# Optimization experiments

Hardware: AMD Instinct MI355X
Metric: run time of the kernel (lower is better)

## Reference

```python
import jax, jax.numpy as jnp
import numpy as np

EPS = 1e-5  # BatchNorm eps (inference-mode BN with running stats)


def bn(x, g, b, m, v):
    # x: [B,C,H,W]; per-channel affine BN (inference)
    inv = jax.lax.rsqrt(v + EPS)
    return (x - m[None, :, None, None]) * (g * inv)[None, :, None, None] + b[None, :, None, None]


def conv1x1(x, w):
    # x: [B,Ci,H,W], w: [Co,Ci,1,1]
    return jnp.einsum('bchw,oc->bohw', x, w[:, :, 0, 0])


def conv3x3(x, w, b):
    out = jax.lax.conv_general_dilated(
        x, w, window_strides=(1, 1), padding=((1, 1), (1, 1)),
        dimension_numbers=('NCHW', 'OIHW', 'NCHW'))
    return out + b[None, :, None, None]


def deform_conv3x3(x, offset, w):
    # x: [B,C,H,W]; offset: [B,18,H,W] with channel 2k = dy_k, 2k+1 = dx_k
    # w: [Co,C,3,3]; stride=1, pad=1, dilation=1, deformable_groups=1
    B, C, H, W = x.shape
    K = 9
    kidx = jnp.arange(K)
    kdy = (kidx // 3 - 1).astype(x.dtype)  # base kernel y offsets in {-1,0,1}
    kdx = (kidx % 3 - 1).astype(x.dtype)
    off = offset.reshape(B, K, 2, H, W)
    gh = jnp.arange(H, dtype=x.dtype)
    gw = jnp.arange(W, dtype=x.dtype)
    # sampling locations [B,K,H,W]
    py = gh[None, None, :, None] + kdy[None, :, None, None] + off[:, :, 0]
    px = gw[None, None, None, :] + kdx[None, :, None, None] + off[:, :, 1]

    y0 = jnp.floor(py)
    x0 = jnp.floor(px)
    wy1 = py - y0
    wx1 = px - x0
    y0i = y0.astype(jnp.int32)
    x0i = x0.astype(jnp.int32)

    xflat = x.reshape(B, C, H * W)

    def gather(yi, xi):
        valid = ((yi >= 0) & (yi < H) & (xi >= 0) & (xi < W))
        idx = (jnp.clip(yi, 0, H - 1) * W + jnp.clip(xi, 0, W - 1)).reshape(B, 1, -1)
        g = jnp.take_along_axis(xflat, idx, axis=2).reshape(B, C, K, H, W)
        return g * valid[:, None].astype(x.dtype)

    sampled = (
        gather(y0i, x0i) * ((1 - wy1) * (1 - wx1))[:, None]
        + gather(y0i, x0i + 1) * ((1 - wy1) * wx1)[:, None]
        + gather(y0i + 1, x0i) * (wy1 * (1 - wx1))[:, None]
        + gather(y0i + 1, x0i + 1) * (wy1 * wx1)[:, None]
    )  # [B,C,K,H,W]
    return jnp.einsum('bckhw,ock->bohw', sampled, w.reshape(w.shape[0], C, K))


def setup_inputs() -> dict:
    key = jax.random.key(0)
    ks = jax.random.split(key, 20)
    B, Cin, H, W = 2, 1024, 64, 64
    Cb, Cout = 256, 1024

    def msra(k, shape):
        fan_out = shape[0] * int(np.prod(shape[2:]))
        return jax.random.normal(k, shape, jnp.float32) * np.sqrt(2.0 / fan_out)

    inp = {
        'x': jax.random.normal(ks[0], (B, Cin, H, W), jnp.float32),
        'w1': msra(ks[1], (Cb, Cin, 1, 1)),
        'g1': jnp.ones((Cb,)), 'b1': jnp.zeros((Cb,)),
        'm1': jax.random.normal(ks[2], (Cb,)) * 0.1,
        'v1': jax.random.uniform(ks[3], (Cb,)) + 0.5,
        # offset conv (small weights so offsets stay in a realistic range)
        'w_off': msra(ks[4], (18, Cb, 3, 3)) * 0.05,
        'b_off': jnp.zeros((18,)),
        'w2': msra(ks[5], (Cb, Cb, 3, 3)),
        'g2': jnp.ones((Cb,)), 'b2': jnp.zeros((Cb,)),
        'm2': jax.random.normal(ks[6], (Cb,)) * 0.1,
        'v2': jax.random.uniform(ks[7], (Cb,)) + 0.5,
        'w3': msra(ks[8], (Cout, Cb, 1, 1)),
        'g3': jnp.ones((Cout,)), 'b3': jnp.zeros((Cout,)),
        'm3': jax.random.normal(ks[9], (Cout,)) * 0.1,
        'v3': jax.random.uniform(ks[10], (Cout,)) + 0.5,
    }
    return inp


def reference(x, w1, g1, b1, m1, v1, w_off, b_off, w2, g2, b2, m2, v2,
              w3, g3, b3, m3, v3):
    out = jax.nn.relu(bn(conv1x1(x, w1), g1, b1, m1, v1))
    offset = conv3x3(out, w_off, b_off)          # [B,18,H,W]
    out = bn(deform_conv3x3(out, offset, w2), g2, b2, m2, v2)
    out = jax.nn.relu(out)
    out = bn(conv1x1(out, w3), g3, b3, m3, v3)
    out = out + x                                 # identity shortcut (Cin==Cout, stride=1)
    return jax.nn.relu(out)
```

## Files before the change

kernel.cpp:

```cpp
#include <hip/hip_runtime.h>
#include <hip/hip_bf16.h>

#define EPSV 1e-5f

typedef __attribute__((ext_vector_type(4))) float f32x4;
typedef __attribute__((ext_vector_type(8))) short bf16x8;
typedef unsigned short u16;
typedef unsigned int u32;

#define AS1(p) ((const __attribute__((address_space(1))) void*)(p))
#define AS3(p) ((__attribute__((address_space(3))) void*)(p))

__device__ __forceinline__ float bf2f(u16 u) {
    union { u32 i; float f; } x; x.i = ((u32)u) << 16; return x.f;
}
__device__ __forceinline__ u16 f2bf(float f) {
    __hip_bfloat16 h = __float2bfloat16(f);
    return *reinterpret_cast<u16*>(&h);
}

__global__ __launch_bounds__(256) void prep_cvt(const float* __restrict__ w1,
                                                const float* __restrict__ w3,
                                                u16* __restrict__ wb1,
                                                u16* __restrict__ wb3) {
    int i = blockIdx.x * 256 + threadIdx.x;
    const float* src; u16* dst; int j;
    if (i < 65536) { src = w1; dst = wb1; j = i; }
    else           { src = w3; dst = wb3; j = i - 65536; }
    float4 v = ((const float4*)src)[j];
    ushort4 o;
    o.x = f2bf(v.x); o.y = f2bf(v.y); o.z = f2bf(v.z); o.w = f2bf(v.w);
    ((ushort4*)dst)[j] = o;
}

__global__ __launch_bounds__(256) void prep_reorg(const float* __restrict__ w_off,
                                                  const float* __restrict__ w2,
                                                  u16* __restrict__ wOffP,
                                                  u16* __restrict__ wb2p,
                                                  u16* __restrict__ zbuf) {
    const int bz = blockIdx.x;
    const int c  = threadIdx.x;
    if (bz == 320) { ((u32*)zbuf)[c] = 0; return; }
    const float* src; u16* dst; int o, O;
    if (bz < 64) { o = bz;      O = 18;  src = w_off; dst = wOffP; }
    else         { o = bz - 64; O = 256; src = w2;    dst = wb2p;  }
#pragma unroll
    for (int k = 0; k < 9; k++) {
        float v = (o < O) ? src[((size_t)(o * 256 + c)) * 9 + k] : 0.f;
        dst[(size_t)o * 2304 + k * 256 + c] = f2bf(v);
    }
}

__global__ __launch_bounds__(256) void cvt_x_T(const float* __restrict__ x,
                                               u16* __restrict__ xbT) {
    __shared__ u16 tile[64][72];
    const int tid = threadIdx.x;
    const int hw0 = blockIdx.x << 6;
    const int c0  = blockIdx.y << 6;
    const int b   = blockIdx.z;
    const int cl  = tid >> 4;
    const int hwl = (tid & 15) << 2;
#pragma unroll
    for (int i = 0; i < 4; i++) {
        const int c = cl + i * 16;
        float4 v = *(const float4*)(x + (((size_t)(b * 1024 + c0 + c)) << 12) + hw0 + hwl);
        tile[hwl + 0][c] = f2bf(v.x);
        tile[hwl + 1][c] = f2bf(v.y);
        tile[hwl + 2][c] = f2bf(v.z);
        tile[hwl + 3][c] = f2bf(v.w);
    }
    __syncthreads();
    const int hw  = tid >> 2;
    const int seg = tid & 3;
    u16* dst = xbT + ((size_t)(b * 4096 + hw0 + hw)) * 1024 + c0 + seg * 16;
    const u16* src = &tile[hw][seg * 16];
#pragma unroll
    for (int q = 0; q < 2; q++)
        *(uint4*)(dst + q * 8) = *(const uint4*)(src + q * 8);
}

#define MFMA8(ASP, BSP)                                                          \
    do {                                                                         \
        bf16x8 a0 = *(const bf16x8*)(ASP);                                       \
        bf16x8 a1 = *(const bf16x8*)((ASP) + 512);                               \
        bf16x8 b0 = *(const bf16x8*)(BSP);                                       \
        bf16x8 b1 = *(const bf16x8*)((BSP) + 512);                               \
        bf16x8 b2 = *(const bf16x8*)((BSP) + 1024);                              \
        bf16x8 b3 = *(const bf16x8*)((BSP) + 1536);                              \
        acc[0][0] = __builtin_amdgcn_mfma_f32_16x16x32_bf16(a0, b0, acc[0][0], 0, 0, 0); \
        acc[0][1] = __builtin_amdgcn_mfma_f32_16x16x32_bf16(a0, b1, acc[0][1], 0, 0, 0); \
        acc[0][2] = __builtin_amdgcn_mfma_f32_16x16x32_bf16(a0, b2, acc[0][2], 0, 0, 0); \
        acc[0][3] = __builtin_amdgcn_mfma_f32_16x16x32_bf16(a0, b3, acc[0][3], 0, 0, 0); \
        acc[1][0] = __builtin_amdgcn_mfma_f32_16x16x32_bf16(a1, b0, acc[1][0], 0, 0, 0); \
        acc[1][1] = __builtin_amdgcn_mfma_f32_16x16x32_bf16(a1, b1, acc[1][1], 0, 0, 0); \
        acc[1][2] = __builtin_amdgcn_mfma_f32_16x16x32_bf16(a1, b2, acc[1][2], 0, 0, 0); \
        acc[1][3] = __builtin_amdgcn_mfma_f32_16x16x32_bf16(a1, b3, acc[1][3], 0, 0, 0); \
    } while (0)

#define WAIT_BAR()                                  \
    do {                                            \
        asm volatile("s_waitcnt vmcnt(3)" ::: "memory"); \
        __builtin_amdgcn_s_barrier();               \
        __builtin_amdgcn_sched_barrier(0);          \
    } while (0)

#define POST_BAR()                                  \
    do {                                            \
        __builtin_amdgcn_s_barrier();               \
        __builtin_amdgcn_sched_barrier(0);          \
    } while (0)

template<int MODE>
__global__ __launch_bounds__(256) void gemm_bn(
    const u16* __restrict__ A, const u16* __restrict__ BT,
    const float* __restrict__ g, const float* __restrict__ bb,
    const float* __restrict__ m, const float* __restrict__ v,
    const float* __restrict__ resid, void* __restrict__ out, int K, int Ksub)
{
    extern __shared__ char sm[];

    const int tid  = threadIdx.x;
    const int lane = tid & 63;
    const int wid  = tid >> 6;
    const int n0 = blockIdx.x << 7;
    const int m0 = blockIdx.y << 6;
    const int kBase = blockIdx.z * Ksub;
    const int wr = wid >> 1, wc = wid & 1;
    const int lr = lane & 15, kg = lane >> 4;

    f32x4 acc[2][4] = {};

    const int arow = tid >> 2, aseg = (tid & 3) << 3;
    const u16* aG  = A  + (size_t)(m0 + arow) * K + kBase + aseg;
    const u16* bG0 = BT + (size_t)(n0 + arow) * K + kBase + aseg;
    const u16* bG1 = BT + (size_t)(n0 + 64 + arow) * K + kBase + aseg;

    char* ldsA0  = sm + wid * 1024;
    char* ldsA1  = sm + 4096  + wid * 1024;
    char* ldsB00 = sm + 8192  + wid * 1024;
    char* ldsB01 = sm + 12288 + wid * 1024;
    char* ldsB10 = sm + 16384 + wid * 1024;
    char* ldsB11 = sm + 20480 + wid * 1024;

    const u16* Asp0 = (const u16*)(sm)         + (wr * 32 + lr) * 32 + kg * 8;
    const u16* Asp1 = (const u16*)(sm + 4096)  + (wr * 32 + lr) * 32 + kg * 8;
    const u16* Bsp0 = (const u16*)(sm + 8192)  + (wc * 64 + lr) * 32 + kg * 8;
    const u16* Bsp1 = (const u16*)(sm + 16384) + (wc * 64 + lr) * 32 + kg * 8;

    float sc[2][4], tc[2][4];
#pragma unroll
    for (int mm = 0; mm < 2; mm++)
#pragma unroll
        for (int r = 0; r < 4; r++) {
            const int o = m0 + wr * 32 + mm * 16 + kg * 4 + r;
            const float s = g[o] * rsqrtf(v[o] + EPSV);
            sc[mm][r] = s;
            tc[mm][r] = bb[o] - m[o] * s;
        }
    asm volatile("s_waitcnt vmcnt(0) lgkmcnt(0)" ::: "memory");
    __builtin_amdgcn_sched_barrier(0);

#define ISSUE_G(LA, LB0, LB1, kt)                                                  \
    do {                                                                           \
        __builtin_amdgcn_global_load_lds(AS1(aG + (kt)),  AS3(LA),  16, 0, 0);     \
        __builtin_amdgcn_global_load_lds(AS1(bG0 + (kt)), AS3(LB0), 16, 0, 0);     \
        __builtin_amdgcn_global_load_lds(AS1(bG1 + (kt)), AS3(LB1), 16, 0, 0);     \
    } while (0)

    const int nT = Ksub >> 5;
    ISSUE_G(ldsA0, ldsB00, ldsB01, 0);
    ISSUE_G(ldsA1, ldsB10, ldsB11, 32);

    for (int t = 0; t < nT; t += 2) {
        WAIT_BAR();
        MFMA8(Asp0, Bsp0);
        POST_BAR();
        { const int kn = (t + 2 < nT ? t + 2 : t) << 5;
          ISSUE_G(ldsA0, ldsB00, ldsB01, kn); }
        WAIT_BAR();
        MFMA8(Asp1, Bsp1);
        POST_BAR();
        { const int kn = (t + 3 < nT ? t + 3 : t + 1) << 5;
          ISSUE_G(ldsA1, ldsB10, ldsB11, kn); }
    }
#undef ISSUE_G

    if (MODE == 1) {
        u32* T32 = (u32*)(sm + 24576);
#pragma unroll
        for (int mm = 0; mm < 2; mm++) {
            const int ol = wr * 32 + mm * 16 + kg * 4;
            const int cw0 = ol >> 1;
#pragma unroll
            for (int j = 0; j < 4; j++) {
                const int nl = wc * 64 + j * 16 + lr;
                const int sw = (nl >> 3) & 3;
                float v0 = acc[mm][j][0] * sc[mm][0] + tc[mm][0];
                float v1 = acc[mm][j][1] * sc[mm][1] + tc[mm][1];
                float v2 = acc[mm][j][2] * sc[mm][2] + tc[mm][2];
                float v3 = acc[mm][j][3] * sc[mm][3] + tc[mm][3];
                v0 = v0 > 0.f ? v0 : 0.f; v1 = v1 > 0.f ? v1 : 0.f;
                v2 = v2 > 0.f ? v2 : 0.f; v3 = v3 > 0.f ? v3 : 0.f;
                uint2 pw;
                pw.x = (u32)f2bf(v0) | ((u32)f2bf(v1) << 16);
                pw.y = (u32)f2bf(v2) | ((u32)f2bf(v3) << 16);
                *(uint2*)&T32[nl * 36 + (cw0 ^ (sw << 2))] = pw;
            }
        }
        __syncthreads();
        const int nl = tid >> 1, half = tid & 1;
        const int sw = (nl >> 3) & 3;
        u16* dst = (u16*)out + (size_t)(n0 + nl) * 256 + m0 + half * 32;
#pragma unroll
        for (int q = 0; q < 4; q++) {
            uint4 val = *(const uint4*)&T32[nl * 36 + ((half * 16 + q * 4) ^ (sw << 2))];
            *(uint4*)(dst + q * 8) = val;
        }
    } else {
        float* T = (float*)(sm + 24576);
#pragma unroll
        for (int mm = 0; mm < 2; mm++) {
            const int ol = wr * 32 + mm * 16 + kg * 4;
#pragma unroll
            for (int j = 0; j < 4; j++) {
                const int nl = wc * 64 + j * 16 + lr;
#pragma unroll
                for (int r = 0; r < 4; r++)
                    T[(ol + r) * 132 + nl] = acc[mm][j][r] * sc[mm][r] + tc[mm][r];
            }
        }
        __syncthreads();
        float* O = (float*)out;
        for (int idx = tid; idx < 2048; idx += 256) {
            const int ol  = idx >> 5;
            const int nl4 = (idx & 31) << 2;
            const int n = n0 + nl4;
            const size_t gidx = ((size_t)(n >> 12) << 22) + ((size_t)(m0 + ol) << 12) + (n & 4095);
            float4 rv = *(const float4*)(resid + gidx);
            float4 ov;
            ov.x = T[ol * 132 + nl4 + 0] + rv.x;
            ov.y = T[ol * 132 + nl4 + 1] + rv.y;
            ov.z = T[ol * 132 + nl4 + 2] + rv.z;
            ov.w = T[ol * 132 + nl4 + 3] + rv.w;
            ov.x = ov.x > 0.f ? ov.x : 0.f;
            ov.y = ov.y > 0.f ? ov.y : 0.f;
            ov.z = ov.z > 0.f ? ov.z : 0.f;
            ov.w = ov.w > 0.f ? ov.w : 0.f;
            *(float4*)(O + gidx) = ov;
        }
    }
}

__global__ __launch_bounds__(256) void gemm_off(
    const u16* __restrict__ A,
    const u16* __restrict__ out1T,
    const u16* __restrict__ zbuf,
    float* __restrict__ offsP)
{
    __shared__ char sm[24576];

    const int tid  = threadIdx.x;
    const int lane = tid & 63;
    const int wid  = tid >> 6;
    const int n0 = blockIdx.x << 7;
    const int kz = blockIdx.y;
    const int wr = wid >> 1, wc = wid & 1;
    const int lr = lane & 15, kg = lane >> 4;

    f32x4 acc[2][4] = {};

    const int arow = tid >> 2, aseg = (tid & 3) << 3;
    const u16* aG = A + (size_t)arow * 2304 + aseg;
    const int nB0 = n0 + arow, nB1 = n0 + 64 + arow;
    const int y0r = (nB0 & 4095) >> 6, x0r = nB0 & 63;
    const int y1r = (nB1 & 4095) >> 6, x1r = nB1 & 63;

    char* ldsA0  = sm + wid * 1024;
    char* ldsA1  = sm + 4096  + wid * 1024;
    char* ldsB00 = sm + 8192  + wid * 1024;
    char* ldsB01 = sm + 12288 + wid * 1024;
    char* ldsB10 = sm + 16384 + wid * 1024;
    char* ldsB11 = sm + 20480 + wid * 1024;

    const u16* Asp0 = (const u16*)(sm)         + (wr * 32 + lr) * 32 + kg * 8;
    const u16* Asp1 = (const u16*)(sm + 4096)  + (wr * 32 + lr) * 32 + kg * 8;
    const u16* Bsp0 = (const u16*)(sm + 8192)  + (wc * 64 + lr) * 32 + kg * 8;
    const u16* Bsp1 = (const u16*)(sm + 16384) + (wc * 64 + lr) * 32 + kg * 8;

#define ISSUE_O(LA, LB0, LB1, kt)                                                  \
    do {                                                                           \
        const int tap = (kt) >> 8, c0 = (kt) & 255;                                \
        const int dy = tap / 3 - 1, dx = tap % 3 - 1;                              \
        const int sh = dy * 64 + dx;                                               \
        const bool vv0 = ((unsigned)(y0r + dy) < 64u) && ((unsigned)(x0r + dx) < 64u); \
        const bool vv1 = ((unsigned)(y1r + dy) < 64u) && ((unsigned)(x1r + dx) < 64u); \
        const u16* s0 = vv0 ? out1T + (size_t)(nB0 + sh) * 256 + c0 + aseg : zbuf + aseg; \
        const u16* s1 = vv1 ? out1T + (size_t)(nB1 + sh) * 256 + c0 + aseg : zbuf + aseg; \
        __builtin_amdgcn_global_load_lds(AS1(aG + (kt)), AS3(LA),  16, 0, 0);      \
        __builtin_amdgcn_global_load_lds(AS1(s0),        AS3(LB0), 16, 0, 0);      \
        __builtin_amdgcn_global_load_lds(AS1(s1),        AS3(LB1), 16, 0, 0);      \
    } while (0)

    const int kBase = kz * 384;
    ISSUE_O(ldsA0, ldsB00, ldsB01, kBase);
    ISSUE_O(ldsA1, ldsB10, ldsB11, kBase + 32);

    for (int t = 0; t < 12; t += 2) {
        WAIT_BAR();
        MFMA8(Asp0, Bsp0);
        POST_BAR();
        { const int kn = kBase + ((t + 2 < 12 ? t + 2 : t) << 5);
          ISSUE_O(ldsA0, ldsB00, ldsB01, kn); }
        WAIT_BAR();
        MFMA8(Asp1, Bsp1);
        POST_BAR();
        { const int kn = kBase + ((t + 3 < 12 ? t + 3 : t + 1) << 5);
          ISSUE_O(ldsA1, ldsB10, ldsB11, kn); }
    }
#undef ISSUE_O

    asm volatile("s_waitcnt vmcnt(0)" ::: "memory");

#pragma unroll
    for (int mm = 0; mm < 2; mm++)
#pragma unroll
        for (int r = 0; r < 4; r++) {
            const int o = wr * 32 + mm * 16 + kg * 4 + r;
            if (o < 18) {
#pragma unroll
                for (int j = 0; j < 4; j++) {
                    const int n = n0 + wc * 64 + j * 16 + lr;
                    offsP[(size_t)kz * 147456 +
                          (((size_t)((n >> 12) * 18 + o)) << 12) + (n & 4095)] =
                        acc[mm][j][r];
                }
            }
        }
}

__global__ __launch_bounds__(256) void reduce_offs(
    const float* __restrict__ offsP,
    const float* __restrict__ b_off,
    float* __restrict__ offs)
{
    const int i = blockIdx.x * 256 + threadIdx.x;
    const int ch = (i >> 10) % 18;
    const float bo = b_off[ch];
    float4 s = make_float4(bo, bo, bo, bo);
#pragma unroll
    for (int kz = 0; kz < 6; kz++) {
        float4 v = ((const float4*)(offsP + (size_t)kz * 147456))[i];
        s.x += v.x; s.y += v.y; s.z += v.z; s.w += v.w;
    }
    ((float4*)offs)[i] = s;
}

__global__ __launch_bounds__(256) void gemm_def(
    const u16* __restrict__ A,
    const u16* __restrict__ out1T,
    const float* __restrict__ offs,
    float* __restrict__ P)
{
    extern __shared__ char sm[];
    char*   ldsA0 = sm;
    char*   ldsA1 = sm + 16384;
    char*   ldsB0 = sm + 32768;
    char*   ldsB1 = sm + 37888;
    int4*   s_ofs = (int4*)(sm + 43008);
    float4* s_w   = (float4*)(sm + 52224);

    const int tid  = threadIdx.x;
    const int lane = tid & 63;
    const int wid  = tid >> 6;
    const int n0 = blockIdx.x << 6;
    const int kz = blockIdx.y;
    const int b  = n0 >> 12;
    const int h  = (n0 >> 6) & 63;
    const int lr = lane & 15, kg = lane >> 4;

    for (int p = tid; p < 576; p += 256) {
        const int nl = p / 9;
        const int t  = p - nl * 9;
        const float dy = offs[(((size_t)(b * 18 + 2 * t)) << 12) + (h << 6) + nl];
        const float dx = offs[(((size_t)(b * 18 + 2 * t + 1)) << 12) + (h << 6) + nl];
        const float py = (float)h + (float)(t / 3 - 1) + dy;
        const float px = (float)nl + (float)(t % 3 - 1) + dx;
        const float y0f = floorf(py), x0f = floorf(px);
        const int y0 = (int)y0f, x0 = (int)x0f;
        const float wy1 = py - y0f, wx1 = px - x0f;
        const float wy0 = 1.f - wy1, wx0 = 1.f - wx1;
        const int y1 = y0 + 1, x1 = x0 + 1;
        const bool vy0 = (y0 >= 0) && (y0 < 64);
        const bool vy1 = (y1 >= 0) && (y1 < 64);
        const bool vx0 = (x0 >= 0) && (x0 < 64);
        const bool vx1 = (x1 >= 0) && (x1 < 64);
        const int cy0 = min(max(y0, 0), 63), cy1 = min(max(y1, 0), 63);
        const int cx0 = min(max(x0, 0), 63), cx1 = min(max(x1, 0), 63);
        const int rb = b << 12;
        int4 o4; float4 w4;
        o4.x = (rb + (cy0 << 6) + cx0) << 9;  w4.x = wy0 * wx0 * ((vy0 && vx0) ? 1.f : 0.f);
        o4.y = (rb + (cy0 << 6) + cx1) << 9;  w4.y = wy0 * wx1 * ((vy0 && vx1) ? 1.f : 0.f);
        o4.z = (rb + (cy1 << 6) + cx0) << 9;  w4.z = wy1 * wx0 * ((vy1 && vx0) ? 1.f : 0.f);
        o4.w = (rb + (cy1 << 6) + cx1) << 9;  w4.w = wy1 * wx1 * ((vy1 && vx1) ? 1.f : 0.f);
        s_ofs[p] = o4; s_w[p] = w4;
    }
    __syncthreads();

    const int nl   = tid >> 2;
    const int cs8  = (tid & 3) << 3;
    const int arow = wid * 64 + (lane >> 2);
    const int ak   = (lane & 3) << 3;
    const int bwOff = nl * 80 + (tid & 3) * 16;
    const char* o1B = (const char*)out1T;

    f32x4 acc[4][4] = {};
    bf16x8 cr0[4], cr1[4];

#define ISSUE_D(BUFI, LA, pt_)                                                     \
    do {                                                                           \
        const int kt_ = ((pt_) >> 2) * 256 + kz * 128 + ((pt_) & 3) * 32;          \
        const u16* ag_ = A + (size_t)arow * 2304 + kt_ + ak;                       \
        __builtin_amdgcn_global_load_lds(AS1(ag_),             AS3(LA + (wid*4+0)*1024), 16, 0, 0); \
        __builtin_amdgcn_global_load_lds(AS1(ag_ + 16 * 2304), AS3(LA + (wid*4+1)*1024), 16, 0, 0); \
        __builtin_amdgcn_global_load_lds(AS1(ag_ + 32 * 2304), AS3(LA + (wid*4+2)*1024), 16, 0, 0); \
        __builtin_amdgcn_global_load_lds(AS1(ag_ + 48 * 2304), AS3(LA + (wid*4+3)*1024), 16, 0, 0); \
        __builtin_amdgcn_sched_barrier(0);                                         \
        const int4 o4_ = s_ofs[nl * 9 + ((pt_) >> 2)];                             \
        const int cb_  = (kz * 128 + ((pt_) & 3) * 32 + cs8) * 2;                  \
        cr##BUFI[0] = *(const bf16x8*)(o1B + o4_.x + cb_);                         \
        cr##BUFI[1] = *(const bf16x8*)(o1B + o4_.y + cb_);                         \
        cr##BUFI[2] = *(const bf16x8*)(o1B + o4_.z + cb_);                         \
        cr##BUFI[3] = *(const bf16x8*)(o1B + o4_.w + cb_);                         \
    } while (0)

#define MFMA16(LA, LB)                                                             \
    do {                                                                           \
        bf16x8 av0 = *(const bf16x8*)((const u16*)(LA) + (wid*64 +  0 + lr)*32 + kg*8); \
        bf16x8 av1 = *(const bf16x8*)((const u16*)(LA) + (wid*64 + 16 + lr)*32 + kg*8); \
        bf16x8 av2 = *(const bf16x8*)((const u16*)(LA) + (wid*64 + 32 + lr)*32 + kg*8); \
        bf16x8 av3 = *(const bf16x8*)((const u16*)(LA) + (wid*64 + 48 + lr)*32 + kg*8); \
        bf16x8 bv0 = *(const bf16x8*)((const char*)(LB) + ( 0 + lr)*80 + kg*16);   \
        bf16x8 bv1 = *(const bf16x8*)((const char*)(LB) + (16 + lr)*80 + kg*16);   \
        bf16x8 bv2 = *(const bf16x8*)((const char*)(LB) + (32 + lr)*80 + kg*16);   \
        bf16x8 bv3 = *(const bf16x8*)((const char*)(LB) + (48 + lr)*80 + kg*16);   \
        acc[0][0] = __builtin_amdgcn_mfma_f32_16x16x32_bf16(av0, bv0, acc[0][0], 0, 0, 0); \
        acc[0][1] = __builtin_amdgcn_mfma_f32_16x16x32_bf16(av0, bv1, acc[0][1], 0, 0, 0); \
        acc[0][2] = __builtin_amdgcn_mfma_f32_16x16x32_bf16(av0, bv2, acc[0][2], 0, 0, 0); \
        acc[0][3] = __builtin_amdgcn_mfma_f32_16x16x32_bf16(av0, bv3, acc[0][3], 0, 0, 0); \
        acc[1][0] = __builtin_amdgcn_mfma_f32_16x16x32_bf16(av1, bv0, acc[1][0], 0, 0, 0); \
        acc[1][1] = __builtin_amdgcn_mfma_f32_16x16x32_bf16(av1, bv1, acc[1][1], 0, 0, 0); \
        acc[1][2] = __builtin_amdgcn_mfma_f32_16x16x32_bf16(av1, bv2, acc[1][2], 0, 0, 0); \
        acc[1][3] = __builtin_amdgcn_mfma_f32_16x16x32_bf16(av1, bv3, acc[1][3], 0, 0, 0); \
        acc[2][0] = __builtin_amdgcn_mfma_f32_16x16x32_bf16(av2, bv0, acc[2][0], 0, 0, 0); \
        acc[2][1] = __builtin_amdgcn_mfma_f32_16x16x32_bf16(av2, bv1, acc[2][1], 0, 0, 0); \
        acc[2][2] = __builtin_amdgcn_mfma_f32_16x16x32_bf16(av2, bv2, acc[2][2], 0, 0, 0); \
        acc[2][3] = __builtin_amdgcn_mfma_f32_16x16x32_bf16(av2, bv3, acc[2][3], 0, 0, 0); \
        acc[3][0] = __builtin_amdgcn_mfma_f32_16x16x32_bf16(av3, bv0, acc[3][0], 0, 0, 0); \
        acc[3][1] = __builtin_amdgcn_mfma_f32_16x16x32_bf16(av3, bv1, acc[3][1], 0, 0, 0); \
        acc[3][2] = __builtin_amdgcn_mfma_f32_16x16x32_bf16(av3, bv2, acc[3][2], 0, 0, 0); \
        acc[3][3] = __builtin_amdgcn_mfma_f32_16x16x32_bf16(av3, bv3, acc[3][3], 0, 0, 0); \
    } while (0)

#define PHASE_D(BUFI, LA, LB, p_, pt_)                                             \
    do {                                                                           \
        const float4 w4_ = s_w[nl * 9 + ((p_) >> 2)];                              \
        bf16x8 pk_;                                                                \
        _Pragma("unroll")                                                          \
        for (int i_ = 0; i_ < 8; i_++) {                                           \
            const float f_ = w4_.x * bf2f((u16)cr##BUFI[0][i_])                    \
                           + w4_.y * bf2f((u16)cr##BUFI[1][i_])                    \
                           + w4_.z * bf2f((u16)cr##BUFI[2][i_])                    \
                           + w4_.w * bf2f((u16)cr##BUFI[3][i_]);                   \
            pk_[i_] = (short)f2bf(f_);                                             \
        }                                                                          \
        *(bf16x8*)((char*)(LB) + bwOff) = pk_;                                     \
        asm volatile("s_waitcnt lgkmcnt(0)" ::: "memory");                         \
        __builtin_amdgcn_s_barrier();                                              \
        __builtin_amdgcn_sched_barrier(0);                                         \
        MFMA16(LA, LB);                                                            \
        __builtin_amdgcn_s_barrier();                                              \
        __builtin_amdgcn_sched_barrier(0);                                         \
        ISSUE_D(BUFI, LA, pt_);                                                    \
    } while (0)

    ISSUE_D(0, ldsA0, 0);
    ISSUE_D(1, ldsA1, 1);

    for (int t = 0; t < 36; t += 2) {
        PHASE_D(0, ldsA0, ldsB0, t,     (t + 2 < 36 ? t + 2 : t));
        PHASE_D(1, ldsA1, ldsB1, t + 1, (t + 3 < 36 ? t + 3 : t + 1));
    }
#undef PHASE_D
#undef MFMA16
#undef ISSUE_D

    asm volatile("s_waitcnt vmcnt(0)" ::: "memory");

    float* Pk = P + (size_t)kz * 2097152;
#pragma unroll
    for (int mf = 0; mf < 4; mf++)
#pragma unroll
        for (int r = 0; r < 4; r++) {
            const int o = wid * 64 + mf * 16 + kg * 4 + r;
#pragma unroll
            for (int nf = 0; nf < 4; nf++) {
                const int n = n0 + nf * 16 + lr;
                Pk[((size_t)o << 13) + n] = acc[mf][nf][r];
            }
        }
}

__global__ __launch_bounds__(256) void reduce_bn(
    const float* __restrict__ P,
    const float* __restrict__ g, const float* __restrict__ bb,
    const float* __restrict__ m, const float* __restrict__ v,
    u16* __restrict__ o2T)
{
    __shared__ u16 tile[64][72];
    const int tid = threadIdx.x;
    const int n0 = blockIdx.x << 6;
    const int m0 = blockIdx.y << 6;

    const int ml = tid >> 2;
    const int ns = (tid & 3) << 4;
    const int o = m0 + ml;
    const float s = g[o] * rsqrtf(v[o] + EPSV);
    const float tcv = bb[o] - m[o] * s;
    const size_t base = ((size_t)o << 13) + n0 + ns;
#pragma unroll
    for (int q = 0; q < 4; q++) {
        float4 a = *(const float4*)(P + base + q * 4);
        float4 b = *(const float4*)(P + 2097152 + base + q * 4);
        float f0 = (a.x + b.x) * s + tcv;
        float f1 = (a.y + b.y) * s + tcv;
        float f2 = (a.z + b.z) * s + tcv;
        float f3 = (a.w + b.w) * s + tcv;
        f0 = f0 > 0.f ? f0 : 0.f; f1 = f1 > 0.f ? f1 : 0.f;
        f2 = f2 > 0.f ? f2 : 0.f; f3 = f3 > 0.f ? f3 : 0.f;
        tile[ns + q * 4 + 0][ml] = f2bf(f0);
        tile[ns + q * 4 + 1][ml] = f2bf(f1);
        tile[ns + q * 4 + 2][ml] = f2bf(f2);
        tile[ns + q * 4 + 3][ml] = f2bf(f3);
    }
    __syncthreads();
    const int nl = tid >> 2, seg = tid & 3;
    u16* dst = o2T + (size_t)(n0 + nl) * 256 + m0 + seg * 16;
    const u16* src = &tile[nl][seg * 16];
#pragma unroll
    for (int q = 0; q < 2; q++)
        *(uint4*)(dst + q * 8) = *(const uint4*)(src + q * 8);
}

extern "C" void kernel_launch(void* const* d_in, const int* in_sizes, int n_in,
                              void* d_out, int out_size, void* d_ws, size_t ws_size,
                              hipStream_t stream) {
    const float* x     = (const float*)d_in[0];
    const float* w1    = (const float*)d_in[1];
    const float* g1    = (const float*)d_in[2];
    const float* b1    = (const float*)d_in[3];
    const float* m1    = (const float*)d_in[4];
    const float* v1    = (const float*)d_in[5];
    const float* w_off = (const float*)d_in[6];
    const float* b_off = (const float*)d_in[7];
    const float* w2    = (const float*)d_in[8];
    const float* g2    = (const float*)d_in[9];
    const float* b2    = (const float*)d_in[10];
    const float* m2    = (const float*)d_in[11];
    const float* v2    = (const float*)d_in[12];
    const float* w3    = (const float*)d_in[13];
    const float* g3    = (const float*)d_in[14];
    const float* b3    = (const float*)d_in[15];
    const float* m3    = (const float*)d_in[16];
    const float* v3    = (const float*)d_in[17];
    float* out = (float*)d_out;

    char* ws = (char*)d_ws;
    u16*  xbT   = (u16*)ws;   ws += (size_t)8192 * 1024 * 2;
    u16*  wb1   = (u16*)ws;   ws += (size_t)256 * 1024 * 2;
    u16*  wb3   = (u16*)ws;   ws += (size_t)1024 * 256 * 2;
    u16*  wOffP = (u16*)ws;   ws += (size_t)64 * 2304 * 2;
    u16*  wb2p  = (u16*)ws;   ws += (size_t)256 * 2304 * 2;
    u16*  zbuf  = (u16*)ws;   ws += (size_t)512 * 2;
    u16*  out1T = (u16*)ws;   ws += (size_t)8192 * 256 * 2;
    float* offsP = (float*)ws; ws += (size_t)6 * 147456 * 4;
    float* offs  = (float*)ws; ws += (size_t)147456 * 4;
    u16*  o2T   = (u16*)ws;   ws += (size_t)8192 * 256 * 2;
    float* P    = (float*)xbT;

    prep_cvt<<<dim3(512), 256, 0, stream>>>(w1, w3, wb1, wb3);
    prep_reorg<<<dim3(321), 256, 0, stream>>>(w_off, w2, wOffP, wb2p, zbuf);
    cvt_x_T<<<dim3(64, 16, 2), 256, 0, stream>>>(x, xbT);

    gemm_bn<1><<<dim3(64, 4), 256, 24576 + 18432, stream>>>(
        wb1, xbT, g1, b1, m1, v1, nullptr, out1T, 1024, 1024);

    gemm_off<<<dim3(64, 6), 256, 0, stream>>>(wOffP, out1T, zbuf, offsP);

    reduce_offs<<<dim3(144), 256, 0, stream>>>(offsP, b_off, offs);

    gemm_def<<<dim3(128, 2), 256, 61440, stream>>>(wb2p, out1T, offs, P);

    reduce_bn<<<dim3(128, 4), 256, 0, stream>>>(P, g2, b2, m2, v2, o2T);

    gemm_bn<2><<<dim3(64, 16), 256, 24576 + 64 * 132 * 4, stream>>>(
        wb3, o2T, g3, b3, m3, v3, x, out, 256, 256);
}
```

Before: 111.8 us.

## Split deformable GEMM K four ways and stage A through registers

The deformable-conv GEMM now splits its K dimension over four blocks instead of two, which doubles the grid, and the BN reduction sums four partial buffers. The A operand is no longer copied straight into LDS with global_load_lds. It is loaded into registers and written to a new K-major LDS layout, in a register-prefetch pipeline that uses one barrier per stage. The goal is more parallelism and better latency hiding, at the cost of a separate, larger partial-sum buffer with more write and read traffic and higher register pressure.

```diff
diff --git a/kernel.cpp b/kernel.cpp
--- a/kernel.cpp
+++ b/kernel.cpp
@@ -365,9 +365,9 @@
     char*   ldsA0 = sm;
     char*   ldsA1 = sm + 16384;
     char*   ldsB0 = sm + 32768;
-    char*   ldsB1 = sm + 37888;
-    int4*   s_ofs = (int4*)(sm + 43008);
-    float4* s_w   = (float4*)(sm + 52224);
+    char*   ldsB1 = sm + 36928;
+    int4*   s_ofs = (int4*)(sm + 41088);
+    float4* s_w   = (float4*)(sm + 50304);
 
     const int tid  = threadIdx.x;
     const int lane = tid & 63;
@@ -379,12 +379,12 @@
     const int lr = lane & 15, kg = lane >> 4;
 
     for (int p = tid; p < 576; p += 256) {
-        const int nl = p / 9;
-        const int t  = p - nl * 9;
-        const float dy = offs[(((size_t)(b * 18 + 2 * t)) << 12) + (h << 6) + nl];
-        const float dx = offs[(((size_t)(b * 18 + 2 * t + 1)) << 12) + (h << 6) + nl];
+        const int nl_ = p / 9;
+        const int t   = p - nl_ * 9;
+        const float dy = offs[(((size_t)(b * 18 + 2 * t)) << 12) + (h << 6) + nl_];
+        const float dx = offs[(((size_t)(b * 18 + 2 * t + 1)) << 12) + (h << 6) + nl_];
         const float py = (float)h + (float)(t / 3 - 1) + dy;
-        const float px = (float)nl + (float)(t % 3 - 1) + dx;
+        const float px = (float)nl_ + (float)(t % 3 - 1) + dx;
         const float y0f = floorf(py), x0f = floorf(px);
         const int y0 = (int)y0f, x0 = (int)x0f;
         const float wy1 = py - y0f, wx1 = px - x0f;
@@ -406,43 +406,62 @@
     }
     __syncthreads();
 
-    const int nl   = tid >> 2;
-    const int cs8  = (tid & 3) << 3;
-    const int arow = wid * 64 + (lane >> 2);
-    const int ak   = (lane & 3) << 3;
-    const int bwOff = nl * 80 + (tid & 3) * 16;
+    const int nl = tid >> 2;
+    const int q  = tid & 3;
+    const u16* aRow = A + (size_t)tid * 2304 + kz * 64;
     const char* o1B = (const char*)out1T;
+    const int cbQ = kz * 128 + q * 16;
 
     f32x4 acc[4][4] = {};
-    bf16x8 cr0[4], cr1[4];
-
-#define ISSUE_D(BUFI, LA, pt_)                                                     \
+    bf16x8 ar0[4], ar1[4], cr0[4], cr1[4];
+
+#define PWC(p_) ((p_) < 18 ? (p_) : 17)
+
+#define LOADR(RI, pt_)                                                             \
     do {                                                                           \
-        const int kt_ = ((pt_) >> 2) * 256 + kz * 128 + ((pt_) & 3) * 32;          \
-        const u16* ag_ = A + (size_t)arow * 2304 + kt_ + ak;                       \
-        __builtin_amdgcn_global_load_lds(AS1(ag_),             AS3(LA + (wid*4+0)*1024), 16, 0, 0); \
-        __builtin_amdgcn_global_load_lds(AS1(ag_ + 16 * 2304), AS3(LA + (wid*4+1)*1024), 16, 0, 0); \
-        __builtin_amdgcn_global_load_lds(AS1(ag_ + 32 * 2304), AS3(LA + (wid*4+2)*1024), 16, 0, 0); \
-        __builtin_amdgcn_global_load_lds(AS1(ag_ + 48 * 2304), AS3(LA + (wid*4+3)*1024), 16, 0, 0); \
-        __builtin_amdgcn_sched_barrier(0);                                         \
-        const int4 o4_ = s_ofs[nl * 9 + ((pt_) >> 2)];                             \
-        const int cb_  = (kz * 128 + ((pt_) & 3) * 32 + cs8) * 2;                  \
-        cr##BUFI[0] = *(const bf16x8*)(o1B + o4_.x + cb_);                         \
-        cr##BUFI[1] = *(const bf16x8*)(o1B + o4_.y + cb_);                         \
-        cr##BUFI[2] = *(const bf16x8*)(o1B + o4_.z + cb_);                         \
-        cr##BUFI[3] = *(const bf16x8*)(o1B + o4_.w + cb_);                         \
+        const int tap_ = (pt_) >> 1, hk_ = (pt_) & 1;                              \
+        const u16* ag_ = aRow + tap_ * 256 + hk_ * 32;                             \
+        ar##RI[0] = *(const bf16x8*)(ag_);                                         \
+        ar##RI[1] = *(const bf16x8*)(ag_ + 8);                                     \
+        ar##RI[2] = *(const bf16x8*)(ag_ + 16);                                    \
+        ar##RI[3] = *(const bf16x8*)(ag_ + 24);                                    \
+        const int4 o4_ = s_ofs[nl * 9 + tap_];                                     \
+        const int cb_ = cbQ + hk_ * 64;                                            \
+        cr##RI[0] = *(const bf16x8*)(o1B + o4_.x + cb_);                           \
+        cr##RI[1] = *(const bf16x8*)(o1B + o4_.y + cb_);                           \
+        cr##RI[2] = *(const bf16x8*)(o1B + o4_.z + cb_);                           \
+        cr##RI[3] = *(const bf16x8*)(o1B + o4_.w + cb_);                           \
+    } while (0)
+
+#define WRITE_SET(RI, LA, LB, pw_)                                                 \
+    do {                                                                           \
+        *(bf16x8*)((LA) + 0 * 4096 + tid * 16) = ar##RI[0];                        \
+        *(bf16x8*)((LA) + 1 * 4096 + tid * 16) = ar##RI[1];                        \
+        *(bf16x8*)((LA) + 2 * 4096 + tid * 16) = ar##RI[2];                        \
+        *(bf16x8*)((LA) + 3 * 4096 + tid * 16) = ar##RI[3];                        \
+        const float4 w4_ = s_w[nl * 9 + ((pw_) >> 1)];                             \
+        bf16x8 pk_;                                                                \
+        _Pragma("unroll")                                                          \
+        for (int i_ = 0; i_ < 8; i_++) {                                           \
+            const float f_ = w4_.x * bf2f((u16)cr##RI[0][i_])                      \
+                           + w4_.y * bf2f((u16)cr##RI[1][i_])                      \
+                           + w4_.z * bf2f((u16)cr##RI[2][i_])                      \
+                           + w4_.w * bf2f((u16)cr##RI[3][i_]);                     \
+            pk_[i_] = (short)f2bf(f_);                                             \
+        }                                                                          \
+        *(bf16x8*)((LB) + q * 1040 + nl * 16) = pk_;                               \
     } while (0)
 
 #define MFMA16(LA, LB)                                                             \
     do {                                                                           \
-        bf16x8 av0 = *(const bf16x8*)((const u16*)(LA) + (wid*64 +  0 + lr)*32 + kg*8); \
-        bf16x8 av1 = *(const bf16x8*)((const u16*)(LA) + (wid*64 + 16 + lr)*32 + kg*8); \
-        bf16x8 av2 = *(const bf16x8*)((const u16*)(LA) + (wid*64 + 32 + lr)*32 + kg*8); \
-        bf16x8 av3 = *(const bf16x8*)((const u16*)(LA) + (wid*64 + 48 + lr)*32 + kg*8); \
-        bf16x8 bv0 = *(const bf16x8*)((const char*)(LB) + ( 0 + lr)*80 + kg*16);   \
-        bf16x8 bv1 = *(const bf16x8*)((const char*)(LB) + (16 + lr)*80 + kg*16);   \
-        bf16x8 bv2 = *(const bf16x8*)((const char*)(LB) + (32 + lr)*80 + kg*16);   \
-        bf16x8 bv3 = *(const bf16x8*)((const char*)(LB) + (48 + lr)*80 + kg*16);   \
+        bf16x8 av0 = *(const bf16x8*)((LA) + kg * 4096 + (wid * 64 +  0 + lr) * 16); \
+        bf16x8 av1 = *(const bf16x8*)((LA) + kg * 4096 + (wid * 64 + 16 + lr) * 16); \
+        bf16x8 av2 = *(const bf16x8*)((LA) + kg * 4096 + (wid * 64 + 32 + lr) * 16); \
+        bf16x8 av3 = *(const bf16x8*)((LA) + kg * 4096 + (wid * 64 + 48 + lr) * 16); \
+        bf16x8 bv0 = *(const bf16x8*)((LB) + kg * 1040 + ( 0 + lr) * 16);          \
+        bf16x8 bv1 = *(const bf16x8*)((LB) + kg * 1040 + (16 + lr) * 16);          \
+        bf16x8 bv2 = *(const bf16x8*)((LB) + kg * 1040 + (32 + lr) * 16);          \
+        bf16x8 bv3 = *(const bf16x8*)((LB) + kg * 1040 + (48 + lr) * 16);          \
         acc[0][0] = __builtin_amdgcn_mfma_f32_16x16x32_bf16(av0, bv0, acc[0][0], 0, 0, 0); \
         acc[0][1] = __builtin_amdgcn_mfma_f32_16x16x32_bf16(av0, bv1, acc[0][1], 0, 0, 0); \
         acc[0][2] = __builtin_amdgcn_mfma_f32_16x16x32_bf16(av0, bv2, acc[0][2], 0, 0, 0); \
@@ -461,40 +480,34 @@
         acc[3][3] = __builtin_amdgcn_mfma_f32_16x16x32_bf16(av3, bv3, acc[3][3], 0, 0, 0); \
     } while (0)
 
-#define PHASE_D(BUFI, LA, LB, p_, pt_)                                             \
-    do {                                                                           \
-        const float4 w4_ = s_w[nl * 9 + ((p_) >> 2)];                              \
-        bf16x8 pk_;                                                                \
-        _Pragma("unroll")                                                          \
-        for (int i_ = 0; i_ < 8; i_++) {                                           \
-            const float f_ = w4_.x * bf2f((u16)cr##BUFI[0][i_])                    \
-                           + w4_.y * bf2f((u16)cr##BUFI[1][i_])                    \
-                           + w4_.z * bf2f((u16)cr##BUFI[2][i_])                    \
-                           + w4_.w * bf2f((u16)cr##BUFI[3][i_]);                   \
-            pk_[i_] = (short)f2bf(f_);                                             \
-        }                                                                          \
-        *(bf16x8*)((char*)(LB) + bwOff) = pk_;                                     \
-        asm volatile("s_waitcnt lgkmcnt(0)" ::: "memory");                         \
-        __builtin_amdgcn_s_barrier();                                              \
-        __builtin_amdgcn_sched_barrier(0);                                         \
-        MFMA16(LA, LB);                                                            \
-        __builtin_amdgcn_s_barrier();                                              \
-        __builtin_amdgcn_sched_barrier(0);                                         \
-        ISSUE_D(BUFI, LA, pt_);                                                    \
-    } while (0)
-
-    ISSUE_D(0, ldsA0, 0);
-    ISSUE_D(1, ldsA1, 1);
-
-    for (int t = 0; t < 36; t += 2) {
-        PHASE_D(0, ldsA0, ldsB0, t,     (t + 2 < 36 ? t + 2 : t));
-        PHASE_D(1, ldsA1, ldsB1, t + 1, (t + 3 < 36 ? t + 3 : t + 1));
-    }
-#undef PHASE_D
+#define END_BAR()                                   \
+    do {                                            \
+        asm volatile("s_waitcnt lgkmcnt(0)" ::: "memory"); \
+        __builtin_amdgcn_s_barrier();               \
+        __builtin_amdgcn_sched_barrier(0);          \
+    } while (0)
+
+    LOADR(0, 0);
+    LOADR(1, 1);
+    WRITE_SET(0, ldsA0, ldsB0, 0);
+    LOADR(0, 2);
+    END_BAR();
+
+    for (int t = 0; t < 18; t += 2) {
+        WRITE_SET(1, ldsA1, ldsB1, PWC(t + 1));
+        LOADR(1, PWC(t + 3));
+        MFMA16(ldsA0, ldsB0);
+        END_BAR();
+        WRITE_SET(0, ldsA0, ldsB0, PWC(t + 2));
+        LOADR(0, PWC(t + 4));
+        MFMA16(ldsA1, ldsB1);
+        END_BAR();
+    }
+#undef END_BAR
 #undef MFMA16
-#undef ISSUE_D
-
-    asm volatile("s_waitcnt vmcnt(0)" ::: "memory");
+#undef WRITE_SET
+#undef LOADR
+#undef PWC
 
     float* Pk = P + (size_t)kz * 2097152;
 #pragma unroll
@@ -528,27 +541,29 @@
     const float tcv = bb[o] - m[o] * s;
     const size_t base = ((size_t)o << 13) + n0 + ns;
 #pragma unroll
-    for (int q = 0; q < 4; q++) {
-        float4 a = *(const float4*)(P + base + q * 4);
-        float4 b = *(const float4*)(P + 2097152 + base + q * 4);
-        float f0 = (a.x + b.x) * s + tcv;
-        float f1 = (a.y + b.y) * s + tcv;
-        float f2 = (a.z + b.z) * s + tcv;
-        float f3 = (a.w + b.w) * s + tcv;
+    for (int qq = 0; qq < 4; qq++) {
+        float4 a = *(const float4*)(P + base + qq * 4);
+        float4 b = *(const float4*)(P + 2097152 + base + qq * 4);
+        float4 c = *(const float4*)(P + 2 * 2097152 + base + qq * 4);
+        float4 d = *(const float4*)(P + 3 * 2097152 + base + qq * 4);
+        float f0 = (a.x + b.x + c.x + d.x) * s + tcv;
+        float f1 = (a.y + b.y + c.y + d.y) * s + tcv;
+        float f2 = (a.z + b.z + c.z + d.z) * s + tcv;
+        float f3 = (a.w + b.w + c.w + d.w) * s + tcv;
         f0 = f0 > 0.f ? f0 : 0.f; f1 = f1 > 0.f ? f1 : 0.f;
         f2 = f2 > 0.f ? f2 : 0.f; f3 = f3 > 0.f ? f3 : 0.f;
-        tile[ns + q * 4 + 0][ml] = f2bf(f0);
-        tile[ns + q * 4 + 1][ml] = f2bf(f1);
-        tile[ns + q * 4 + 2][ml] = f2bf(f2);
-        tile[ns + q * 4 + 3][ml] = f2bf(f3);
+        tile[ns + qq * 4 + 0][ml] = f2bf(f0);
+        tile[ns + qq * 4 + 1][ml] = f2bf(f1);
+        tile[ns + qq * 4 + 2][ml] = f2bf(f2);
+        tile[ns + qq * 4 + 3][ml] = f2bf(f3);
     }
     __syncthreads();
     const int nl = tid >> 2, seg = tid & 3;
     u16* dst = o2T + (size_t)(n0 + nl) * 256 + m0 + seg * 16;
     const u16* src = &tile[nl][seg * 16];
 #pragma unroll
-    for (int q = 0; q < 2; q++)
-        *(uint4*)(dst + q * 8) = *(const uint4*)(src + q * 8);
+    for (int qq = 0; qq < 2; qq++)
+        *(uint4*)(dst + qq * 8) = *(const uint4*)(src + qq * 8);
 }
 
 extern "C" void kernel_launch(void* const* d_in, const int* in_sizes, int n_in,
@@ -585,7 +600,7 @@
     float* offsP = (float*)ws; ws += (size_t)6 * 147456 * 4;
     float* offs  = (float*)ws; ws += (size_t)147456 * 4;
     u16*  o2T   = (u16*)ws;   ws += (size_t)8192 * 256 * 2;
-    float* P    = (float*)xbT;
+    float* P    = (float*)ws;  ws += (size_t)4 * 2097152 * 4;
 
     prep_cvt<<<dim3(512), 256, 0, stream>>>(w1, w3, wb1, wb3);
     prep_reorg<<<dim3(321), 256, 0, stream>>>(w_off, w2, wOffP, wb2p, zbuf);
@@ -598,7 +613,7 @@
 
     reduce_offs<<<dim3(144), 256, 0, stream>>>(offsP, b_off, offs);
 
-    gemm_def<<<dim3(128, 2), 256, 61440, stream>>>(wb2p, out1T, offs, P);
+    gemm_def<<<dim3(128, 4), 256, 59520, stream>>>(wb2p, out1T, offs, P);
 
     reduce_bn<<<dim3(128, 4), 256, 0, stream>>>(P, g2, b2, m2, v2, o2T);
 
```

Result: no change. 113.1 us (+1.1%).
